# Kernel optimization log

Measured on AMD Instinct MI355X. Metric: run time of the kernel, lower is better.

The kernel has to match this reference:

```python
import jax, jax.numpy as jnp
import numpy as np

PD = 3                      # spatial feature dim (z, y, x)
HB = 1024                   # hash base per lattice coordinate
HOFF = 512                  # offset: lattice coords assumed in [-512, 511]
FILL = np.int32(2**31 - 1)  # sentinel for padded hash slots
EPS = 2.220446049250313e-16 # np.finfo('float').eps as in the torch module

def _elev_mat():
    # Embedding onto hyperplane sum(x)=0 with std-dev scale factors
    # (canonical permutohedral-lattice elevation, Adams et al.).
    E = np.zeros((PD + 1, PD), np.float32)
    E[0] = 1.0
    for i in range(1, PD + 1):
        E[i, i - 1] = -i
        E[i, i:] = 1.0
    inv_std = np.sqrt(2.0 / 3.0) * (PD + 1)
    scale = inv_std / np.sqrt(np.arange(1, PD + 1) * np.arange(2, PD + 2))
    return (E * scale[None, :]).astype(np.float32)

_EMAT = _elev_mat()
_IU = np.triu(np.ones((PD + 1, PD + 1), bool), 1)   # j > i
_IL = np.tril(np.ones((PD + 1, PD + 1), bool), -1)  # j < i

def _hash(k):  # (..., PD) int32 -> (...,) int32, injective for |coord| < 512
    return ((k[..., 0] + HOFF) * HB + (k[..., 1] + HOFF)) * HB + (k[..., 2] + HOFF)

def permutohedral(values, features):
    """Splat-blur-slice Gaussian filter. values (N,VD), features (N,PD)."""
    N, VD = values.shape
    elevated = features @ jnp.asarray(_EMAT).T                  # (N, PD+1)
    # nearest remainder-0 lattice point (nearest multiple of PD+1, ties -> down)
    v = elevated / (PD + 1)
    up, down = jnp.ceil(v), jnp.floor(v)
    rem0 = jnp.where(up - v < v - down, up, down) * (PD + 1)
    diff = elevated - rem0
    lt = diff[:, :, None] < diff[:, None, :]
    le = diff[:, :, None] <= diff[:, None, :]
    rank = (lt & _IU).sum(-1) + (le & _IL).sum(-1)              # (N, PD+1) int32
    rank = rank + jnp.round(rem0.sum(-1) / (PD + 1)).astype(rank.dtype)[:, None]
    shift = jnp.where(rank < 0, PD + 1, 0) + jnp.where(rank > PD, -(PD + 1), 0)
    rank = rank + shift
    rem0 = rem0 + shift.astype(rem0.dtype)
    # barycentric coordinates inside the enclosing simplex
    t = (elevated - rem0) / (PD + 1)                            # (N, PD+1)
    ohA = jax.nn.one_hot(PD - rank, PD + 2, dtype=values.dtype)
    ohB = jax.nn.one_hot(PD + 1 - rank, PD + 2, dtype=values.dtype)
    b = (ohA * t[..., None]).sum(1) - (ohB * t[..., None]).sum(1)
    b = b.at[:, 0].add(1.0 + b[:, PD + 1])
    bary = b[:, :PD + 1]                                        # (N, PD+1)
    # keys of the PD+1 simplex vertices (first PD coords; last is implied)
    rem0i = rem0[:, :PD].astype(jnp.int32)
    ranki = rank[:, :PD].astype(jnp.int32)
    r = jnp.arange(PD + 1, dtype=jnp.int32)[None, :, None]
    keys = rem0i[:, None, :] + jnp.where(ranki[:, None, :] >= PD + 1 - r, r - (PD + 1), r)  # (N,PD+1,PD)
    h = _hash(keys).reshape(-1)                                 # (N*(PD+1),)
    M = h.shape[0]
    uh, inv = jnp.unique(h, size=M, fill_value=FILL, return_inverse=True)
    inv = inv.reshape(-1)
    # splat
    contrib = (values[:, None, :] * bary[:, :, None]).reshape(M, VD)
    lat = jax.ops.segment_sum(contrib, inv, num_segments=M)     # (M, VD)
    # decode unique keys from the (invertible) hash
    k2 = uh % HB - HOFF
    tq = uh // HB
    k1 = tq % HB - HOFF
    k0 = tq // HB - HOFF
    ukeys = jnp.stack([k0, k1, k2], -1).astype(jnp.int32)       # (M, PD)
    valid = (uh != FILL)[:, None]
    # blur with [0.5, 1, 0.5] along each of the PD+1 lattice directions
    def lookup(nk, lat_):
        nh = _hash(nk)
        idx = jnp.clip(jnp.searchsorted(uh, nh), 0, M - 1)
        ok = (uh[idx] == nh)[:, None]
        return jnp.where(ok, lat_[idx], 0.0)
    for j in range(PD + 1):
        o = np.ones(PD, np.int32)
        if j < PD:
            o[j] = -PD
        o = jnp.asarray(o)
        lat = jnp.where(valid, lat + 0.5 * (lookup(ukeys + o, lat) + lookup(ukeys - o, lat)), 0.0)
    # slice
    alpha = 1.0 / (1.0 + 2.0 ** (-PD))
    return alpha * jnp.einsum('nr,nrv->nv', bary, lat[inv.reshape(-1, PD + 1)])

def spatial_features(image, v_gamma, sigma_gamma):
    _, d, h, w = image.shape
    z = jnp.arange(d, dtype=jnp.float32)[:, None, None]
    y = jnp.arange(h, dtype=jnp.float32)[None, :, None]
    x = jnp.arange(w, dtype=jnp.float32)[None, None, :]
    zz = v_gamma[0] * jnp.broadcast_to(z, (d, h, w)) / sigma_gamma[0]
    xx = v_gamma[1] * jnp.broadcast_to(x, (d, h, w)) / sigma_gamma[1]
    yy = v_gamma[2] * jnp.broadcast_to(y, (d, h, w)) / sigma_gamma[2]
    return jnp.stack([zz, yy, xx], axis=3)                      # (d,h,w,3)

def setup_inputs() -> dict:
    key = jax.random.key(0)
    k1, k2 = jax.random.split(key)
    C, D, H, W = 4, 64, 128, 128
    return {
        'input_': jax.random.normal(k1, (C, D, H, W), jnp.float32),
        'image': jax.random.normal(k2, (1, D, H, W), jnp.float32),
        'v_gamma': jnp.ones((3,), jnp.float32),       # nn.Parameter init [1,1,1]
        'sigma_gamma': 5.0 * jnp.ones((3,), jnp.float32),
    }

def reference(input_, image, v_gamma, sigma_gamma):
    C, d, h, w = input_.shape
    N = d * h * w
    feats = spatial_features(image, v_gamma, sigma_gamma).reshape(N, PD)
    # filter q and the all-ones normalizer in one pass (linear per channel)
    vals = jnp.concatenate([input_.reshape(C, N).T, jnp.ones((N, 1), jnp.float32)], axis=1)
    out = permutohedral(vals, feats)
    q = out[:, :C].T.reshape(C, d, h, w)
    norm = out[:, C].reshape(1, d, h, w)
    return q * (1.0 / (norm + EPS))
```

## Files before the change

### kernel.cpp

```cpp
#include <hip/hip_runtime.h>


#define DD    64
#define HHH   128
#define WWW   128
#define NPTS  (DD * HHH * WWW)
#define LATN  (1 << 17)
#define SH_BITS 10
#define SHSZ (1 << SH_BITS)

__device__ __forceinline__ int encK(int K0, int K1, int K2) {
    return ((K2 >> 2) << 12) | ((K1 >> 2) << 7) | ((K0 >> 2) << 2) | (K0 & 3);
}

__device__ __forceinline__ void pl_geom(int z, int y, int x,
                                        const float* __restrict__ vg,
                                        const float* __restrict__ sg,
                                        int* didx, float* bout) {
    float f0 = vg[0] * (float)z / sg[0];
    float f1 = vg[2] * (float)y / sg[2];
    float f2 = vg[1] * (float)x / sg[1];

    const float m00 = (float)2.3094010767585034;
    const float m01 = (float)1.3333333333333333;
    const float m02 = (float)0.9428090415820634;
    const float m21 = (float)-2.6666666666666665;
    const float m32 = (float)-2.8284271247461903;

    float e[4];
    e[0] =  m00 * f0 + m01 * f1 + m02 * f2;
    e[1] = -m00 * f0 + m01 * f1 + m02 * f2;
    e[2] =  m21 * f1 + m02 * f2;
    e[3] =  m32 * f2;

    float rem0[4];
    int sumr = 0;
    #pragma unroll
    for (int i = 0; i < 4; ++i) {
        float v = e[i] * 0.25f;
        float up = ceilf(v), dn = floorf(v);
        float rr = ((up - v) < (v - dn)) ? up : dn;
        rem0[i] = rr * 4.0f;
        sumr += (int)rem0[i];
    }
    sumr /= 4;

    float diff[4];
    #pragma unroll
    for (int i = 0; i < 4; ++i) diff[i] = e[i] - rem0[i];
    int rank[4] = {0, 0, 0, 0};
    #pragma unroll
    for (int i = 0; i < 4; ++i)
        #pragma unroll
        for (int j = i + 1; j < 4; ++j) {
            if (diff[i] < diff[j]) rank[i]++; else rank[j]++;
        }

    #pragma unroll
    for (int i = 0; i < 4; ++i) {
        rank[i] += sumr;
        if (rank[i] < 0)      { rank[i] += 4; rem0[i] += 4.0f; }
        else if (rank[i] > 3) { rank[i] -= 4; rem0[i] -= 4.0f; }
    }

    float b[5] = {0.f, 0.f, 0.f, 0.f, 0.f};
    #pragma unroll
    for (int i = 0; i < 4; ++i) {
        float t = (e[i] - rem0[i]) * 0.25f;
        b[3 - rank[i]] += t;
        b[4 - rank[i]] -= t;
    }
    b[0] += 1.0f + b[4];

    int k0 = (int)rem0[0], k1 = (int)rem0[1], k2 = (int)rem0[2];
    #pragma unroll
    for (int r = 0; r < 4; ++r) {
        int o0 = (rank[0] >= 4 - r) ? (r - 4) : r;
        int o1 = (rank[1] >= 4 - r) ? (r - 4) : r;
        int o2 = (rank[2] >= 4 - r) ? (r - 4) : r;
        int K0 = (k0 + o0 + 16) & 127;
        int K1 = (k1 + o1 + 48) & 127;
        int K2 = (k2 + o2 + 88) & 127;
        didx[r] = encK(K0, K1, K2);
        bout[r] = b[r];
    }
}

__device__ __forceinline__ void pl_emit(int key, const float* a,
                                        int* skey, float (*sacc)[5],
                                        float* __restrict__ lat,
                                        unsigned char* __restrict__ exists) {
    unsigned idx = ((unsigned)key * 2654435761u) >> (32 - SH_BITS);
    int probes = 0;
    bool inlds = true;
    for (;;) {
        int cur = skey[idx];
        if (cur == key) break;
        if (cur == -1) {
            cur = atomicCAS(&skey[idx], -1, key);
            if (cur == -1 || cur == key) break;
        }
        idx = (idx + 1) & (SHSZ - 1);
        if (++probes >= SHSZ) { inlds = false; break; }
    }
    if (inlds) {
        #pragma unroll
        for (int c = 0; c < 5; ++c) atomicAdd(&sacc[idx][c], a[c]);
    } else {
        float* L = lat + (size_t)key * 5;
        #pragma unroll
        for (int c = 0; c < 5; ++c) atomicAdd(L + c, a[c]);
        exists[key] = 1;
    }
}

__global__ __launch_bounds__(512, 6)
void pl_splat(const float* __restrict__ vals, const float* __restrict__ vg,
              const float* __restrict__ sg, float* __restrict__ lat,
              unsigned char* __restrict__ exists) {
    __shared__ int   skey[SHSZ];
    __shared__ float sacc[SHSZ][5];
    for (int i = threadIdx.x; i < SHSZ; i += 512) {
        skey[i] = -1;
        #pragma unroll
        for (int c = 0; c < 5; ++c) sacc[i][c] = 0.f;
    }
    __syncthreads();

    int bt = blockIdx.x;
    int lx = threadIdx.x & 15;
    int ly = (threadIdx.x >> 4) & 7;
    int lz = threadIdx.x >> 7;
    int x0 = ((bt & 3) << 5) + (lx << 1);
    int y  = (((bt >> 2) & 15) << 3) + ly;
    int z  = ((bt >> 6) << 2) + lz;
    int n0 = (z << 14) + (y << 7) + x0;

    float2 c0 = *(const float2*)(vals + n0);
    float2 c1 = *(const float2*)(vals + NPTS + n0);
    float2 c2 = *(const float2*)(vals + 2 * NPTS + n0);
    float2 c3 = *(const float2*)(vals + 3 * NPTS + n0);

    int ckey[4];
    float acc[4][5];
    {
        int didx[4]; float b[4];
        pl_geom(z, y, x0, vg, sg, didx, b);
        #pragma unroll
        for (int r = 0; r < 4; ++r) {
            ckey[r] = didx[r];
            float w = b[r];
            acc[r][0] = w * c0.x; acc[r][1] = w * c1.x;
            acc[r][2] = w * c2.x; acc[r][3] = w * c3.x;
            acc[r][4] = w;
        }
    }
    {
        int didx[4]; float b[4];
        pl_geom(z, y, x0 + 1, vg, sg, didx, b);
        #pragma unroll
        for (int r = 0; r < 4; ++r) {
            float w = b[r];
            if (didx[r] == ckey[r]) {
                acc[r][0] += w * c0.y; acc[r][1] += w * c1.y;
                acc[r][2] += w * c2.y; acc[r][3] += w * c3.y;
                acc[r][4] += w;
            } else {
                pl_emit(ckey[r], acc[r], skey, sacc, lat, exists);
                ckey[r] = didx[r];
                acc[r][0] = w * c0.y; acc[r][1] = w * c1.y;
                acc[r][2] = w * c2.y; acc[r][3] = w * c3.y;
                acc[r][4] = w;
            }
        }
    }
    #pragma unroll
    for (int r = 0; r < 4; ++r)
        pl_emit(ckey[r], acc[r], skey, sacc, lat, exists);

    __syncthreads();

    int rot = (blockIdx.x * 131) & (SHSZ - 1);
    for (int ii = threadIdx.x; ii < SHSZ; ii += 512) {
        int i = (ii + rot) & (SHSZ - 1);
        int key = skey[i];
        if (key < 0) continue;
        exists[key] = 1;
        float* L = lat + (size_t)key * 5;
        #pragma unroll
        for (int c = 0; c < 5; ++c) atomicAdd(L + c, sacc[i][c]);
    }
}

__global__ __launch_bounds__(256)
void pl_blur(const float* __restrict__ lin, float* __restrict__ lout,
             const unsigned char* __restrict__ exists,
             int d0, int d1, int d2) {
    int didx = blockIdx.x * 256 + threadIdx.x;
    if (didx >= LATN) return;
    if (!exists[didx]) return;
    int r  = didx & 3;
    int K0 = (((didx >> 2)  & 31) << 2) | r;
    int K1 = (((didx >> 7)  & 31) << 2) | r;
    int K2 = (((didx >> 12) & 31) << 2) | r;
    float acc[5];
    const float* S = lin + (size_t)didx * 5;
    #pragma unroll
    for (int c = 0; c < 5; ++c) acc[c] = S[c];
    #pragma unroll
    for (int sgn = 0; sgn < 2; ++sgn) {
        int a0 = sgn ? -d0 : d0;
        int a1 = sgn ? -d1 : d1;
        int a2 = sgn ? -d2 : d2;
        int P0 = K0 + a0, P1 = K1 + a1, P2 = K2 + a2;
        if (((unsigned)P0 < 128u) & ((unsigned)P1 < 128u) & ((unsigned)P2 < 128u)) {
            const float* L = lin + (size_t)encK(P0, P1, P2) * 5;
            #pragma unroll
            for (int c = 0; c < 5; ++c) acc[c] += 0.5f * L[c];
        }
    }
    float* O = lout + (size_t)didx * 5;
    #pragma unroll
    for (int c = 0; c < 5; ++c) O[c] = acc[c];
}

__global__ __launch_bounds__(256)
void pl_slice(const float* __restrict__ vg, const float* __restrict__ sg,
              const float* __restrict__ lat, float* __restrict__ out) {
    int n = blockIdx.x * 256 + threadIdx.x;
    if (n >= NPTS) return;
    int z = n >> 14;
    int y = (n >> 7) & 127;
    int x = n & 127;
    int didx[4]; float b[4];
    pl_geom(z, y, x, vg, sg, didx, b);
    float a0 = 0.f, a1 = 0.f, a2 = 0.f, a3 = 0.f, a4 = 0.f;
    #pragma unroll
    for (int r = 0; r < 4; ++r) {
        float w = b[r];
        const float* L = lat + (size_t)didx[r] * 5;
        a0 += w * L[0]; a1 += w * L[1]; a2 += w * L[2]; a3 += w * L[3]; a4 += w * L[4];
    }
    const float alpha = (float)(1.0 / 1.125);
    float norm = alpha * a4 + (float)2.220446049250313e-16;
    float invn = 1.0f / norm;
    out[n]            = (alpha * a0) * invn;
    out[NPTS + n]     = (alpha * a1) * invn;
    out[2 * NPTS + n] = (alpha * a2) * invn;
    out[3 * NPTS + n] = (alpha * a3) * invn;
}

extern "C" void kernel_launch(void* const* d_in, const int* in_sizes, int n_in,
                              void* d_out, int out_size, void* d_ws, size_t ws_size,
                              hipStream_t stream) {
    const float* input = (const float*)d_in[0];
    const float* vg = (const float*)d_in[2];
    const float* sg = (const float*)d_in[3];
    float* out = (float*)d_out;

    char* ws = (char*)d_ws;
    size_t off = 0;
    float* lat0 = (float*)(ws + off);            off += (size_t)LATN * 5 * 4;
    float* lat1 = (float*)(ws + off);            off += (size_t)LATN * 5 * 4;
    unsigned char* exists = (unsigned char*)(ws + off); off += LATN;

    hipMemsetAsync(lat0, 0, (size_t)LATN * 5 * 4, stream);
    hipMemsetAsync(lat1, 0, (size_t)LATN * 5 * 4, stream);
    hipMemsetAsync(exists, 0, LATN, stream);

    pl_splat<<<1024, dim3(512), 0, stream>>>(input, vg, sg, lat0, exists);

    const int offs[4][3] = {{-3, 1, 1}, {1, -3, 1}, {1, 1, -3}, {1, 1, 1}};
    float* bufs[2] = {lat0, lat1};
    for (int j = 0; j < 4; ++j) {
        pl_blur<<<LATN / 256, dim3(256), 0, stream>>>(bufs[j & 1], bufs[(j & 1) ^ 1],
                                                      exists,
                                                      offs[j][0], offs[j][1], offs[j][2]);
    }
    pl_slice<<<NPTS / 256, dim3(256), 0, stream>>>(vg, sg, lat0, out);
}
```

Before: 186.8 us.

## Privatize splat lattice into four copies and blur over compacted worklist

Splat now writes into four private lattice copies selected by block index, which spreads contention on global atomics, and each block covers four x points per thread with float4 loads, halving the block count. Occupied lattice keys are claimed with atomicExch and appended to a worklist, so the blur kernels loop over only occupied entries with a small grid instead of scanning the full lattice. The first blur pass sums the four copies. Neighbours that were never written are skipped rather than read, and the lattice buffers are zeroed with a single memset. In exchange the memset is larger, the worklist order is random, and the blur uses only 64 blocks, so parallelism may be limited.

New measurement: 191.2 us. 1.02x slower.

```diff
diff --git a/kernel.cpp b/kernel.cpp
--- a/kernel.cpp
+++ b/kernel.cpp
@@ -6,8 +6,10 @@
 #define WWW   128
 #define NPTS  (DD * HHH * WWW)
 #define LATN  (1 << 17)
+#define LATF  (LATN * 5)
 #define SH_BITS 10
 #define SHSZ (1 << SH_BITS)
+#define BLURBLK 64
 
 __device__ __forceinline__ int encK(int K0, int K1, int K2) {
     return ((K2 >> 2) << 12) | ((K1 >> 2) << 7) | ((K0 >> 2) << 2) | (K0 & 3);
@@ -86,10 +88,19 @@
     }
 }
 
+__device__ __forceinline__ void pl_claim(int key, unsigned int* __restrict__ exists,
+                                         int* __restrict__ wcnt, int* __restrict__ wl) {
+    if (atomicExch(&exists[key], 1u) == 0u) {
+        int p = atomicAdd(wcnt, 1);
+        wl[p] = key;
+    }
+}
+
 __device__ __forceinline__ void pl_emit(int key, const float* a,
                                         int* skey, float (*sacc)[5],
-                                        float* __restrict__ lat,
-                                        unsigned char* __restrict__ exists) {
+                                        float* __restrict__ latc,
+                                        unsigned int* __restrict__ exists,
+                                        int* __restrict__ wcnt, int* __restrict__ wl) {
     unsigned idx = ((unsigned)key * 2654435761u) >> (32 - SH_BITS);
     int probes = 0;
     bool inlds = true;
@@ -107,17 +118,18 @@
         #pragma unroll
         for (int c = 0; c < 5; ++c) atomicAdd(&sacc[idx][c], a[c]);
     } else {
-        float* L = lat + (size_t)key * 5;
+        float* L = latc + (size_t)key * 5;
         #pragma unroll
         for (int c = 0; c < 5; ++c) atomicAdd(L + c, a[c]);
-        exists[key] = 1;
-    }
-}
-
-__global__ __launch_bounds__(512, 6)
+        pl_claim(key, exists, wcnt, wl);
+    }
+}
+
+__global__ __launch_bounds__(512, 4)
 void pl_splat(const float* __restrict__ vals, const float* __restrict__ vg,
-              const float* __restrict__ sg, float* __restrict__ lat,
-              unsigned char* __restrict__ exists) {
+              const float* __restrict__ sg, float* __restrict__ latc,
+              unsigned int* __restrict__ exists,
+              int* __restrict__ wcnt, int* __restrict__ wl) {
     __shared__ int   skey[SHSZ];
     __shared__ float sacc[SHSZ][5];
     for (int i = threadIdx.x; i < SHSZ; i += 512) {
@@ -127,19 +139,26 @@
     }
     __syncthreads();
 
+    float* mycopy = latc + (size_t)(blockIdx.x & 3) * LATF;
+
     int bt = blockIdx.x;
-    int lx = threadIdx.x & 15;
-    int ly = (threadIdx.x >> 4) & 7;
+    int xs = threadIdx.x & 7;
+    int ly = (threadIdx.x >> 3) & 15;
     int lz = threadIdx.x >> 7;
-    int x0 = ((bt & 3) << 5) + (lx << 1);
-    int y  = (((bt >> 2) & 15) << 3) + ly;
-    int z  = ((bt >> 6) << 2) + lz;
+    int xsl = ((xs & 3) << 1) | (xs >> 2);
+    int x0 = ((bt & 3) << 5) + (xsl << 2);
+    int y  = (((bt >> 2) & 7) << 4) + ly;
+    int z  = ((bt >> 5) << 2) + lz;
     int n0 = (z << 14) + (y << 7) + x0;
 
-    float2 c0 = *(const float2*)(vals + n0);
-    float2 c1 = *(const float2*)(vals + NPTS + n0);
-    float2 c2 = *(const float2*)(vals + 2 * NPTS + n0);
-    float2 c3 = *(const float2*)(vals + 3 * NPTS + n0);
+    float4 q0 = *(const float4*)(vals + n0);
+    float4 q1 = *(const float4*)(vals + NPTS + n0);
+    float4 q2 = *(const float4*)(vals + 2 * NPTS + n0);
+    float4 q3 = *(const float4*)(vals + 3 * NPTS + n0);
+    float ch0[4] = {q0.x, q0.y, q0.z, q0.w};
+    float ch1[4] = {q1.x, q1.y, q1.z, q1.w};
+    float ch2[4] = {q2.x, q2.y, q2.z, q2.w};
+    float ch3[4] = {q3.x, q3.y, q3.z, q3.w};
 
     int ckey[4];
     float acc[4][5];
@@ -150,33 +169,34 @@
         for (int r = 0; r < 4; ++r) {
             ckey[r] = didx[r];
             float w = b[r];
-            acc[r][0] = w * c0.x; acc[r][1] = w * c1.x;
-            acc[r][2] = w * c2.x; acc[r][3] = w * c3.x;
+            acc[r][0] = w * ch0[0]; acc[r][1] = w * ch1[0];
+            acc[r][2] = w * ch2[0]; acc[r][3] = w * ch3[0];
             acc[r][4] = w;
         }
     }
-    {
+    #pragma unroll
+    for (int p = 1; p < 4; ++p) {
         int didx[4]; float b[4];
-        pl_geom(z, y, x0 + 1, vg, sg, didx, b);
+        pl_geom(z, y, x0 + p, vg, sg, didx, b);
         #pragma unroll
         for (int r = 0; r < 4; ++r) {
             float w = b[r];
             if (didx[r] == ckey[r]) {
-                acc[r][0] += w * c0.y; acc[r][1] += w * c1.y;
-                acc[r][2] += w * c2.y; acc[r][3] += w * c3.y;
+                acc[r][0] += w * ch0[p]; acc[r][1] += w * ch1[p];
+                acc[r][2] += w * ch2[p]; acc[r][3] += w * ch3[p];
                 acc[r][4] += w;
             } else {
-                pl_emit(ckey[r], acc[r], skey, sacc, lat, exists);
+                pl_emit(ckey[r], acc[r], skey, sacc, mycopy, exists, wcnt, wl);
                 ckey[r] = didx[r];
-                acc[r][0] = w * c0.y; acc[r][1] = w * c1.y;
-                acc[r][2] = w * c2.y; acc[r][3] = w * c3.y;
+                acc[r][0] = w * ch0[p]; acc[r][1] = w * ch1[p];
+                acc[r][2] = w * ch2[p]; acc[r][3] = w * ch3[p];
                 acc[r][4] = w;
             }
         }
     }
     #pragma unroll
     for (int r = 0; r < 4; ++r)
-        pl_emit(ckey[r], acc[r], skey, sacc, lat, exists);
+        pl_emit(ckey[r], acc[r], skey, sacc, mycopy, exists, wcnt, wl);
 
     __syncthreads();
 
@@ -185,43 +205,60 @@
         int i = (ii + rot) & (SHSZ - 1);
         int key = skey[i];
         if (key < 0) continue;
-        exists[key] = 1;
-        float* L = lat + (size_t)key * 5;
+        pl_claim(key, exists, wcnt, wl);
+        float* L = mycopy + (size_t)key * 5;
         #pragma unroll
         for (int c = 0; c < 5; ++c) atomicAdd(L + c, sacc[i][c]);
     }
 }
 
 __global__ __launch_bounds__(256)
-void pl_blur(const float* __restrict__ lin, float* __restrict__ lout,
-             const unsigned char* __restrict__ exists,
-             int d0, int d1, int d2) {
-    int didx = blockIdx.x * 256 + threadIdx.x;
-    if (didx >= LATN) return;
-    if (!exists[didx]) return;
-    int r  = didx & 3;
-    int K0 = (((didx >> 2)  & 31) << 2) | r;
-    int K1 = (((didx >> 7)  & 31) << 2) | r;
-    int K2 = (((didx >> 12) & 31) << 2) | r;
-    float acc[5];
-    const float* S = lin + (size_t)didx * 5;
-    #pragma unroll
-    for (int c = 0; c < 5; ++c) acc[c] = S[c];
-    #pragma unroll
-    for (int sgn = 0; sgn < 2; ++sgn) {
-        int a0 = sgn ? -d0 : d0;
-        int a1 = sgn ? -d1 : d1;
-        int a2 = sgn ? -d2 : d2;
-        int P0 = K0 + a0, P1 = K1 + a1, P2 = K2 + a2;
-        if (((unsigned)P0 < 128u) & ((unsigned)P1 < 128u) & ((unsigned)P2 < 128u)) {
-            const float* L = lin + (size_t)encK(P0, P1, P2) * 5;
+void pl_blur(const unsigned int* __restrict__ exists,
+             const int* __restrict__ wl, const int* __restrict__ wcnt,
+             const float* __restrict__ in, float* __restrict__ out,
+             int d0, int d1, int d2, int first) {
+    int cnt = *wcnt;
+    for (int i = blockIdx.x * 256 + threadIdx.x; i < cnt; i += BLURBLK * 256) {
+        int didx = wl[i];
+        int r  = didx & 3;
+        int K0 = (((didx >> 2)  & 31) << 2) | r;
+        int K1 = (((didx >> 7)  & 31) << 2) | r;
+        int K2 = (((didx >> 12) & 31) << 2) | r;
+        float a[5];
+        size_t o = (size_t)didx * 5;
+        if (first) {
             #pragma unroll
-            for (int c = 0; c < 5; ++c) acc[c] += 0.5f * L[c];
-        }
-    }
-    float* O = lout + (size_t)didx * 5;
-    #pragma unroll
-    for (int c = 0; c < 5; ++c) O[c] = acc[c];
+            for (int c = 0; c < 5; ++c)
+                a[c] = in[o + c] + in[LATF + o + c] +
+                       in[2 * LATF + o + c] + in[3 * LATF + o + c];
+        } else {
+            #pragma unroll
+            for (int c = 0; c < 5; ++c) a[c] = in[o + c];
+        }
+        #pragma unroll
+        for (int sgn = 0; sgn < 2; ++sgn) {
+            int P0 = K0 + (sgn ? -d0 : d0);
+            int P1 = K1 + (sgn ? -d1 : d1);
+            int P2 = K2 + (sgn ? -d2 : d2);
+            if (((unsigned)P0 < 128u) & ((unsigned)P1 < 128u) & ((unsigned)P2 < 128u)) {
+                int nk = encK(P0, P1, P2);
+                if (exists[nk]) {
+                    size_t no = (size_t)nk * 5;
+                    if (first) {
+                        #pragma unroll
+                        for (int c = 0; c < 5; ++c)
+                            a[c] += 0.5f * (in[no + c] + in[LATF + no + c] +
+                                            in[2 * LATF + no + c] + in[3 * LATF + no + c]);
+                    } else {
+                        #pragma unroll
+                        for (int c = 0; c < 5; ++c) a[c] += 0.5f * in[no + c];
+                    }
+                }
+            }
+        }
+        #pragma unroll
+        for (int c = 0; c < 5; ++c) out[o + c] = a[c];
+    }
 }
 
 __global__ __launch_bounds__(256)
@@ -259,23 +296,22 @@
     float* out = (float*)d_out;
 
     char* ws = (char*)d_ws;
-    size_t off = 0;
-    float* lat0 = (float*)(ws + off);            off += (size_t)LATN * 5 * 4;
-    float* lat1 = (float*)(ws + off);            off += (size_t)LATN * 5 * 4;
-    unsigned char* exists = (unsigned char*)(ws + off); off += LATN;
-
-    hipMemsetAsync(lat0, 0, (size_t)LATN * 5 * 4, stream);
-    hipMemsetAsync(lat1, 0, (size_t)LATN * 5 * 4, stream);
-    hipMemsetAsync(exists, 0, LATN, stream);
-
-    pl_splat<<<1024, dim3(512), 0, stream>>>(input, vg, sg, lat0, exists);
-
-    const int offs[4][3] = {{-3, 1, 1}, {1, -3, 1}, {1, 1, -3}, {1, 1, 1}};
-    float* bufs[2] = {lat0, lat1};
-    for (int j = 0; j < 4; ++j) {
-        pl_blur<<<LATN / 256, dim3(256), 0, stream>>>(bufs[j & 1], bufs[(j & 1) ^ 1],
-                                                      exists,
-                                                      offs[j][0], offs[j][1], offs[j][2]);
-    }
-    pl_slice<<<NPTS / 256, dim3(256), 0, stream>>>(vg, sg, lat0, out);
-}
+    float* latc = (float*)ws;
+    unsigned int* exists = (unsigned int*)(latc + (size_t)4 * LATF);
+    int* wcnt = (int*)(exists + LATN);
+    int*   wl = (int*)(wcnt + 64);
+    float* A  = (float*)(wl + LATN);
+    float* B  = A + LATF;
+
+    size_t zbytes = (size_t)4 * LATF * 4 + (size_t)LATN * 4 + 256;
+    hipMemsetAsync(ws, 0, zbytes, stream);
+
+    pl_splat<<<512, dim3(512), 0, stream>>>(input, vg, sg, latc, exists, wcnt, wl);
+
+    pl_blur<<<BLURBLK, dim3(256), 0, stream>>>(exists, wl, wcnt, latc, A, -3, 1, 1, 1);
+    pl_blur<<<BLURBLK, dim3(256), 0, stream>>>(exists, wl, wcnt, A, B, 1, -3, 1, 0);
+    pl_blur<<<BLURBLK, dim3(256), 0, stream>>>(exists, wl, wcnt, B, A, 1, 1, -3, 0);
+    pl_blur<<<BLURBLK, dim3(256), 0, stream>>>(exists, wl, wcnt, A, B, 1, 1, 1, 0);
+
+    pl_slice<<<NPTS / 256, dim3(256), 0, stream>>>(vg, sg, B, out);
+}
```
